# Performance work log

Measured on AMD Instinct MI355X. Metric: run time of the kernel, lower is better.

Reference implementation:

```python
import jax, jax.numpy as jnp
import numpy as np

B, C, H, W = 8, 256, 64, 64
D = C // 8  # qk proj dim = 32
R = C // 8  # channel-SE reduction dim = 32

def setup_inputs() -> dict:
    key = jax.random.key(0)
    ks = jax.random.split(key, 10)
    s = lambda *sh: 1.0 / np.sqrt(sh[-1])
    return {
        'x':  jax.random.normal(ks[0], (B, C, H, W), jnp.float32),
        'Wq': jax.random.normal(ks[1], (D, C), jnp.float32) * s(D, C),
        'bq': jnp.zeros((D,), jnp.float32),
        'Wk': jax.random.normal(ks[2], (D, C), jnp.float32) * s(D, C),
        'bk': jnp.zeros((D,), jnp.float32),
        'Wv': jax.random.normal(ks[3], (C, C), jnp.float32) * s(C, C),
        'bv': jnp.zeros((C,), jnp.float32),
        'gamma': jnp.ones((1,), jnp.float32),
        'W1': jax.random.normal(ks[4], (R, 2 * C), jnp.float32) * s(R, 2 * C),
        'W2': jax.random.normal(ks[5], (C, R), jnp.float32) * s(C, R),
        'lamb': jnp.ones((1,), jnp.float32),
    }

def reference(x, Wq, bq, Wk, bk, Wv, bv, gamma, W1, W2, lamb):
    b, c, h, w = x.shape
    n = h * w
    xf = x.reshape(b, c, n)  # [B,C,N]
    # --- spatial self-attention (1x1 convs == matmuls over channel dim) ---
    q = jnp.einsum('dc,bcn->bnd', Wq, xf) + bq            # [B,N,D]
    k = jnp.einsum('dc,bcn->bdn', Wk, xf) + bk[:, None]   # [B,D,N]
    attn = jax.nn.softmax(jnp.einsum('bnd,bdm->bnm', q, k), axis=-1)  # [B,N,N]
    v = jnp.einsum('dc,bcn->bdn', Wv, xf) + bv[:, None]   # [B,C,N]
    # out[b,c,m] = sum_n v[b,c,n] * attn[b,m,n]  (torch: bmm(v, attn^T))
    sp = jnp.einsum('bcn,bmn->bcm', v, attn).reshape(b, c, h, w)
    sp = gamma * sp
    # --- channel SE-gate ---
    mean = jnp.mean(xf, axis=-1)                # [B,C]
    std = jnp.std(xf, axis=-1, ddof=1)          # torch.std uses unbiased (ddof=1)
    inp = jnp.concatenate([mean, std], axis=1)  # [B,2C]
    a = jax.nn.sigmoid(jax.nn.relu(inp @ W1.T) @ W2.T)  # [B,C]
    ch = lamb * a[:, :, None, None] * x
    return sp + ch + x
```

## Files before the change

### kernel.cpp

```cpp
#include <hip/hip_runtime.h>
#include <hip/hip_bf16.h>

#define Bb 8
#define Cc 256
#define Nn 4096
#define Dd 32

typedef short bf16x8 __attribute__((ext_vector_type(8)));
typedef short bf16x4 __attribute__((ext_vector_type(4)));
typedef float f32x4 __attribute__((ext_vector_type(4)));
typedef unsigned int u32;

__device__ __forceinline__ void glds16(const void* g, void* l) {
    __builtin_amdgcn_global_load_lds(
        (const __attribute__((address_space(1))) unsigned int*)g,
        (__attribute__((address_space(3))) unsigned int*)l, 16, 0, 0);
}

__device__ __forceinline__ u32 pkbf16(float a, float b) {
    return ((u32)__bfloat16_as_ushort(__float2bfloat16(b)) << 16) |
           (u32)__bfloat16_as_ushort(__float2bfloat16(a));
}

__global__ __launch_bounds__(256) void convt_kernel(
    const float* __restrict__ x, __hip_bfloat16* __restrict__ x_t,
    float* __restrict__ sum_ws, float* __restrict__ sumsq_ws)
{
    __shared__ __hip_bfloat16 tile[64][68];
    const int n0 = blockIdx.x * 64, c0 = blockIdx.y * 64, b = blockIdx.z;
    const int t = threadIdx.x;

#pragma unroll
    for (int i = 0; i < 4; i++) {
        int id = i * 256 + t;
        int row = id >> 4, col4 = id & 15;
        float4 v = *(const float4*)(x + ((size_t)(b * Cc + c0 + row)) * Nn + n0 + col4 * 4);
        bf16x4 bv;
        bv[0] = __bfloat16_as_short(__float2bfloat16(v.x));
        bv[1] = __bfloat16_as_short(__float2bfloat16(v.y));
        bv[2] = __bfloat16_as_short(__float2bfloat16(v.z));
        bv[3] = __bfloat16_as_short(__float2bfloat16(v.w));
        *(bf16x4*)((void*)&tile[row][col4 * 4]) = bv;
        float ls  = v.x + v.y + v.z + v.w;
        float ls2 = v.x * v.x + v.y * v.y + v.z * v.z + v.w * v.w;
        ls  += __shfl_xor(ls, 1, 16);  ls2 += __shfl_xor(ls2, 1, 16);
        ls  += __shfl_xor(ls, 2, 16);  ls2 += __shfl_xor(ls2, 2, 16);
        ls  += __shfl_xor(ls, 4, 16);  ls2 += __shfl_xor(ls2, 4, 16);
        ls  += __shfl_xor(ls, 8, 16);  ls2 += __shfl_xor(ls2, 8, 16);
        if ((t & 15) == 0) {
            atomicAdd(&sum_ws[b * Cc + c0 + row], ls);
            atomicAdd(&sumsq_ws[b * Cc + c0 + row], ls2);
        }
    }
    __syncthreads();
#pragma unroll
    for (int i = 0; i < 2; i++) {
        int id = i * 256 + t;
        int nl = id >> 3, cg = id & 7;
        bf16x8 o;
#pragma unroll
        for (int j = 0; j < 8; j++) o[j] = __bfloat16_as_short(tile[cg * 8 + j][nl]);
        *(bf16x8*)(x_t + ((size_t)(b * Nn + n0 + nl)) * Cc + c0 + cg * 8) = o;
    }
}

__global__ __launch_bounds__(256) void wconv_kernel(
    const float* __restrict__ Wq, const float* __restrict__ Wk, const float* __restrict__ Wv,
    __hip_bfloat16* __restrict__ w_bf)
{
    const int ct = blockIdx.x;
    const int t = threadIdx.x;
#pragma unroll
    for (int i = 0; i < 8; i++) {
        int g = i * 256 + t;
        int row = g >> 5, c8 = g & 31;
        int c0 = c8 * 8;
        int grow = ct * 64 + row;
        const float* src;
        if (grow < 32)       src = Wq + (size_t)grow * Cc + c0;
        else if (grow < 64)  src = Wk + (size_t)(grow - 32) * Cc + c0;
        else                 src = Wv + (size_t)(grow - 64) * Cc + c0;
        float4 v0 = *(const float4*)src;
        float4 v1 = *(const float4*)(src + 4);
        bf16x8 o;
        o[0] = __bfloat16_as_short(__float2bfloat16(v0.x));
        o[1] = __bfloat16_as_short(__float2bfloat16(v0.y));
        o[2] = __bfloat16_as_short(__float2bfloat16(v0.z));
        o[3] = __bfloat16_as_short(__float2bfloat16(v0.w));
        o[4] = __bfloat16_as_short(__float2bfloat16(v1.x));
        o[5] = __bfloat16_as_short(__float2bfloat16(v1.y));
        o[6] = __bfloat16_as_short(__float2bfloat16(v1.z));
        o[7] = __bfloat16_as_short(__float2bfloat16(v1.w));
        int kchunk = c0 >> 5, qd = (c0 & 31) >> 3, cg = row >> 4, rl = row & 15;
        *(bf16x8*)(w_bf + ((size_t)ct * 32 + kchunk * 4 + cg) * 512 + (qd * 16 + rl) * 8) = o;
    }
}

__global__ __launch_bounds__(256, 2) void proj_kernel(
    const __hip_bfloat16* __restrict__ x_t, const __hip_bfloat16* __restrict__ w_bf,
    const float* __restrict__ bq, const float* __restrict__ bk, const float* __restrict__ bv,
    __hip_bfloat16* __restrict__ q_ws, __hip_bfloat16* __restrict__ k_ws,
    __hip_bfloat16* __restrict__ v_ws)
{
    __shared__ __hip_bfloat16 ldsX[32 * 512];
    __shared__ __hip_bfloat16 ldsW[32 * 512];

    const int n0 = blockIdx.x * 64;
    const int ct = blockIdx.y;
    const int b  = blockIdx.z;
    const int t = threadIdx.x;
    const int w = t >> 6, lane = t & 63, quad = lane >> 4, l15 = lane & 15;

#pragma unroll
    for (int j = 0; j < 8; j++) {
        int idx = w * 8 + j;
        int kchunk = idx >> 2, ngrp = idx & 3;
        glds16(x_t + ((size_t)(b * Nn + n0 + ngrp * 16 + l15)) * Cc + kchunk * 32 + quad * 8,
               ldsX + idx * 512);
        glds16(w_bf + ((size_t)ct * 32 + idx) * 512 + lane * 8, ldsW + idx * 512);
    }
    __syncthreads();

    f32x4 acc[4];
#pragma unroll
    for (int cg = 0; cg < 4; cg++) {
        int gcol = ct * 64 + cg * 16 + l15;
        float bias = (gcol < 32) ? bq[gcol] : (gcol < 64 ? bk[gcol - 32] : bv[gcol - 64]);
        acc[cg] = (f32x4){bias, bias, bias, bias};
    }

#pragma unroll
    for (int kchunk = 0; kchunk < 8; kchunk++) {
        bf16x8 a = *(const bf16x8*)(ldsX + ((kchunk * 4 + w) * 64 + lane) * 8);
#pragma unroll
        for (int cg = 0; cg < 4; cg++) {
            bf16x8 bw = *(const bf16x8*)(ldsW + ((kchunk * 4 + cg) * 64 + lane) * 8);
            acc[cg] = __builtin_amdgcn_mfma_f32_16x16x32_bf16(a, bw, acc[cg], 0, 0, 0);
        }
    }

#pragma unroll
    for (int cg = 0; cg < 4; cg++) {
        int gcol = ct * 64 + cg * 16 + l15;
        int nb = n0 + w * 16 + quad * 4;
        if (gcol < 64) {
            __hip_bfloat16* dst = (gcol < 32) ? q_ws : k_ws;
            int d = gcol & 31;
#pragma unroll
            for (int r = 0; r < 4; r++)
                dst[((size_t)(b * Nn + nb + r)) * Dd + d] = __float2bfloat16(acc[cg][r]);
        } else {
            int c = gcol - 64;
            bf16x4 o;
#pragma unroll
            for (int r = 0; r < 4; r++) o[r] = __bfloat16_as_short(__float2bfloat16(acc[cg][r]));
            *(bf16x4*)(v_ws + ((size_t)(b * Cc + c)) * Nn + nb) = o;
        }
    }
}

__global__ __launch_bounds__(256) void gate_kernel(
    const float* __restrict__ sum_ws, const float* __restrict__ sumsq_ws,
    const float* __restrict__ W1, const float* __restrict__ W2,
    const float* __restrict__ lamb, float* __restrict__ coef)
{
    int b = blockIdx.x;
    __shared__ float inp[2 * Cc];
    __shared__ float h[32];
    int t = threadIdx.x;
    float s  = sum_ws[b * Cc + t];
    float s2 = sumsq_ws[b * Cc + t];
    float m   = s / Nn;
    float var = (s2 - (float)Nn * m * m) / (float)(Nn - 1);
    inp[t]      = m;
    inp[Cc + t] = sqrtf(fmaxf(var, 0.f));
    __syncthreads();
    if (t < 32) {
        float a = 0.f;
        for (int i = 0; i < 2 * Cc; i++) a += W1[t * (2 * Cc) + i] * inp[i];
        h[t] = fmaxf(a, 0.f);
    }
    __syncthreads();
    float g = 0.f;
#pragma unroll
    for (int r = 0; r < 32; r++) g += W2[t * 32 + r] * h[r];
    float a = 1.f / (1.f + __expf(-g));
    coef[b * Cc + t] = 1.f + lamb[0] * a;
}

__global__ __launch_bounds__(512, 2) void attn_kernel(
    const __hip_bfloat16* __restrict__ q_ws, const __hip_bfloat16* __restrict__ k_ws,
    const __hip_bfloat16* __restrict__ v_ws, const float* __restrict__ coef,
    const float* __restrict__ x, const float* __restrict__ gamma_p,
    float* __restrict__ out)
{
    extern __shared__ __hip_bfloat16 smem[];
    __hip_bfloat16* vbuf0 = smem;
    __hip_bfloat16* vbuf1 = smem + 16384;
    __hip_bfloat16* kbuf0 = smem + 32768;
    __hip_bfloat16* kbuf1 = smem + 36864;

    const int b  = blockIdx.x & 7;
    const int m0 = (blockIdx.x >> 3) * 128;
    const int t = threadIdx.x;
    const int w = t >> 6, lane = t & 63, quad = lane >> 4, l15 = lane & 15;
    const int p = w >> 2, pw = w & 3;

    const bf16x8 aq0 = *(const bf16x8*)(q_ws + ((size_t)(b * Nn + m0 + (2 * pw)     * 16 + l15)) * Dd + quad * 8);
    const bf16x8 aq1 = *(const bf16x8*)(q_ws + ((size_t)(b * Nn + m0 + (2 * pw + 1) * 16 + l15)) * Dd + quad * 8);

    const __hip_bfloat16* vsrc[4];
#pragma unroll
    for (int j = 0; j < 4; j++) {
        int idx = w * 4 + j;
        int ch = idx >> 4, tc = idx & 15;
        vsrc[j] = v_ws + ((size_t)(b * Cc + tc * 16 + l15)) * Nn + ch * 32 + quad * 8;
    }
    const int sl15 = (l15 & 3) | ((l15 & 4) << 1) | ((l15 & 8) >> 1);
    const __hip_bfloat16* ksrc = k_ws + ((size_t)(b * Nn + w * 16 + sl15)) * Dd + quad * 8;

#pragma unroll
    for (int j = 0; j < 4; j++) glds16(vsrc[j], vbuf0 + (w * 4 + j) * 512);
    glds16(ksrc, kbuf0 + w * 512);
    __syncthreads();

    f32x4 acc[2][16];
#pragma unroll
    for (int i = 0; i < 2; i++)
#pragma unroll
        for (int j = 0; j < 16; j++) acc[i][j] = (f32x4){0.f, 0.f, 0.f, 0.f};
    float lsum0 = 0.f, lsum1 = 0.f;

    const int NIT = Nn / 64;

    u32 pc0[2][2], pc1[2][2];
#pragma unroll
    for (int j = 0; j < 2; j++) {
        bf16x8 ak = *(const bf16x8*)(kbuf0 + ((2 * p + j) * 64 + lane) * 8);
        f32x4 s0 = __builtin_amdgcn_mfma_f32_16x16x32_bf16(ak, aq0, (f32x4){0.f,0.f,0.f,0.f}, 0, 0, 0);
        f32x4 s1 = __builtin_amdgcn_mfma_f32_16x16x32_bf16(ak, aq1, (f32x4){0.f,0.f,0.f,0.f}, 0, 0, 0);
        float a0 = __expf(s0[0]), a1 = __expf(s0[1]), a2 = __expf(s0[2]), a3 = __expf(s0[3]);
        lsum0 += (a0 + a1) + (a2 + a3);
        pc0[j][0] = pkbf16(a0, a1); pc0[j][1] = pkbf16(a2, a3);
        float b0 = __expf(s1[0]), b1 = __expf(s1[1]), b2 = __expf(s1[2]), b3 = __expf(s1[3]);
        lsum1 += (b0 + b1) + (b2 + b3);
        pc1[j][0] = pkbf16(b0, b1); pc1[j][1] = pkbf16(b2, b3);
    }

    for (int it = 0; it < NIT; it++) {
        if (it + 1 < NIT) {
            __hip_bfloat16* vn = ((it + 1) & 1) ? vbuf1 : vbuf0;
#pragma unroll
            for (int j = 0; j < 4; j++)
                glds16(vsrc[j] + (size_t)(it + 1) * 64, vn + (w * 4 + j) * 512);
        }
        if ((it & 1) == 0 && it + 2 < NIT) {
            int sl = (it >> 1) + 1;
            glds16(ksrc + (size_t)(sl * 128) * Dd, ((sl & 1) ? kbuf1 : kbuf0) + w * 512);
        }

        auto g0 = __builtin_amdgcn_permlane32_swap(pc0[0][0], pc0[1][0], false, false);
        auto g1 = __builtin_amdgcn_permlane32_swap(pc0[0][1], pc0[1][1], false, false);
        auto h0 = __builtin_amdgcn_permlane32_swap(pc1[0][0], pc1[1][0], false, false);
        auto h1 = __builtin_amdgcn_permlane32_swap(pc1[0][1], pc1[1][1], false, false);
        union { u32 uw[4]; bf16x8 v; } bp0, bp1;
        bp0.uw[0] = g0[0]; bp0.uw[1] = g1[0]; bp0.uw[2] = g0[1]; bp0.uw[3] = g1[1];
        bp1.uw[0] = h0[0]; bp1.uw[1] = h1[0]; bp1.uw[2] = h0[1]; bp1.uw[3] = h1[1];

        u32 pn0[2][2], pn1[2][2];
        const int itn = (it + 1 < NIT) ? it + 1 : it;
        const __hip_bfloat16* kbn = (((itn >> 1) & 1) ? kbuf1 : kbuf0) + (itn & 1) * 2048;
        float nls0 = 0.f, nls1 = 0.f;
#pragma unroll
        for (int j = 0; j < 2; j++) {
            bf16x8 ak = *(const bf16x8*)(kbn + ((2 * p + j) * 64 + lane) * 8);
            f32x4 s0 = __builtin_amdgcn_mfma_f32_16x16x32_bf16(ak, aq0, (f32x4){0.f,0.f,0.f,0.f}, 0, 0, 0);
            f32x4 s1 = __builtin_amdgcn_mfma_f32_16x16x32_bf16(ak, aq1, (f32x4){0.f,0.f,0.f,0.f}, 0, 0, 0);
            float a0 = __expf(s0[0]), a1 = __expf(s0[1]), a2 = __expf(s0[2]), a3 = __expf(s0[3]);
            nls0 += (a0 + a1) + (a2 + a3);
            pn0[j][0] = pkbf16(a0, a1); pn0[j][1] = pkbf16(a2, a3);
            float b0 = __expf(s1[0]), b1 = __expf(s1[1]), b2 = __expf(s1[2]), b3 = __expf(s1[3]);
            nls1 += (b0 + b1) + (b2 + b3);
            pn1[j][0] = pkbf16(b0, b1); pn1[j][1] = pkbf16(b2, b3);
        }
        if (it + 1 < NIT) { lsum0 += nls0; lsum1 += nls1; }

        const __hip_bfloat16* vb = (it & 1) ? vbuf1 : vbuf0;
#pragma unroll
        for (int cf = 0; cf < 16; cf++) {
            bf16x8 av = *(const bf16x8*)(vb + ((p * 16 + cf) * 64 + lane) * 8);
            acc[0][cf] = __builtin_amdgcn_mfma_f32_16x16x32_bf16(av, bp0.v, acc[0][cf], 0, 0, 0);
            acc[1][cf] = __builtin_amdgcn_mfma_f32_16x16x32_bf16(av, bp1.v, acc[1][cf], 0, 0, 0);
        }

#pragma unroll
        for (int j = 0; j < 2; j++)
#pragma unroll
            for (int k = 0; k < 2; k++) { pc0[j][k] = pn0[j][k]; pc1[j][k] = pn1[j][k]; }

        __syncthreads();
    }

    float* lex = (float*)(smem + 32768);
    lex[w * 128 + lane]      = lsum0;
    lex[w * 128 + 64 + lane] = lsum1;
    f32x4* exv = (f32x4*)smem;
#pragma unroll
    for (int mfi = 0; mfi < 2; mfi++) {
        __syncthreads();
        if (p == 0) {
#pragma unroll
            for (int j = 0; j < 8; j++) exv[(w * 8 + j) * 64 + lane] = acc[mfi][8 + j];
        } else {
#pragma unroll
            for (int j = 0; j < 8; j++) exv[(w * 8 + j) * 64 + lane] = acc[mfi][j];
        }
        __syncthreads();
        if (p == 0) {
#pragma unroll
            for (int j = 0; j < 8; j++) acc[mfi][j] += exv[((w ^ 4) * 8 + j) * 64 + lane];
        } else {
#pragma unroll
            for (int j = 0; j < 8; j++) acc[mfi][8 + j] += exv[((w ^ 4) * 8 + j) * 64 + lane];
        }
        if (mfi == 0) {
            lsum0 += lex[(w ^ 4) * 128 + lane];
            lsum1 += lex[(w ^ 4) * 128 + 64 + lane];
        }
    }

    lsum0 += __shfl_xor(lsum0, 16); lsum0 += __shfl_xor(lsum0, 32);
    lsum1 += __shfl_xor(lsum1, 16); lsum1 += __shfl_xor(lsum1, 32);
    const float g = gamma_p[0];
    const float inv0 = g / lsum0, inv1 = g / lsum1;

    if (p == 0) {
#pragma unroll
        for (int j = 0; j < 8; j++) {
#pragma unroll
            for (int r = 0; r < 4; r++) {
                int c = j * 16 + quad * 4 + r;
                float cfv = coef[b * Cc + c];
                size_t base = ((size_t)(b * Cc + c)) * Nn + m0 + (2 * pw) * 16 + l15;
                out[base]      = acc[0][j][r] * inv0 + cfv * x[base];
                out[base + 16] = acc[1][j][r] * inv1 + cfv * x[base + 16];
            }
        }
    } else {
#pragma unroll
        for (int j = 0; j < 8; j++) {
#pragma unroll
            for (int r = 0; r < 4; r++) {
                int c = (8 + j) * 16 + quad * 4 + r;
                float cfv = coef[b * Cc + c];
                size_t base = ((size_t)(b * Cc + c)) * Nn + m0 + (2 * pw) * 16 + l15;
                out[base]      = acc[0][8 + j][r] * inv0 + cfv * x[base];
                out[base + 16] = acc[1][8 + j][r] * inv1 + cfv * x[base + 16];
            }
        }
    }
}

extern "C" void kernel_launch(void* const* d_in, const int* in_sizes, int n_in,
                              void* d_out, int out_size, void* d_ws, size_t ws_size,
                              hipStream_t stream) {
    const float* x     = (const float*)d_in[0];
    const float* Wq    = (const float*)d_in[1];
    const float* bq    = (const float*)d_in[2];
    const float* Wk    = (const float*)d_in[3];
    const float* bk    = (const float*)d_in[4];
    const float* Wv    = (const float*)d_in[5];
    const float* bv    = (const float*)d_in[6];
    const float* gamma = (const float*)d_in[7];
    const float* W1    = (const float*)d_in[8];
    const float* W2    = (const float*)d_in[9];
    const float* lamb  = (const float*)d_in[10];
    float* out = (float*)d_out;

    char* ws = (char*)d_ws;
    __hip_bfloat16* q_ws = (__hip_bfloat16*)ws;
    __hip_bfloat16* k_ws = (__hip_bfloat16*)(ws + (2u  << 20));
    __hip_bfloat16* v_ws = (__hip_bfloat16*)(ws + (4u  << 20));
    __hip_bfloat16* x_t  = (__hip_bfloat16*)(ws + (20u << 20));
    float* sum_ws   = (float*)(ws + (36u << 20));
    float* sumsq_ws = sum_ws + Bb * Cc;
    float* coef     = sumsq_ws + Bb * Cc;
    __hip_bfloat16* w_bf = (__hip_bfloat16*)(ws + (37u << 20));

    (void)hipFuncSetAttribute((const void*)attn_kernel,
                              hipFuncAttributeMaxDynamicSharedMemorySize, 81920);

    hipMemsetAsync(sum_ws, 0, 2 * Bb * Cc * sizeof(float), stream);
    wconv_kernel<<<5, 256, 0, stream>>>(Wq, Wk, Wv, w_bf);
    convt_kernel<<<dim3(Nn / 64, Cc / 64, Bb), 256, 0, stream>>>(x, x_t, sum_ws, sumsq_ws);
    proj_kernel<<<dim3(Nn / 64, 5, Bb), 256, 0, stream>>>(x_t, w_bf, bq, bk, bv, q_ws, k_ws, v_ws);
    gate_kernel<<<Bb, 256, 0, stream>>>(sum_ws, sumsq_ws, W1, W2, lamb, coef);
    attn_kernel<<<256, 512, 81920, stream>>>(q_ws, k_ws, v_ws, coef, x, gamma, out);
}
```

Baseline: 245.7 us.

## Triple-buffer V/K tiles in attention loop with prefetch distance two

The attention kernel's V and K shared-memory staging moves from double to triple buffering with rotating pointers, so global-to-LDS loads are issued two iterations ahead. The per-iteration __syncthreads is replaced by an explicit s_waitcnt vmcnt(4) plus s_barrier, so the most recent prefetch can stay in flight across the barrier. The aim is to hide global memory latency behind the MFMA work. In exchange, dynamic LDS per block rises from 80 KB to 120 KB, which rules out two resident blocks per CU, and correctness now depends on the hand-written waitcnt counting.

```diff
diff --git a/kernel.cpp b/kernel.cpp
--- a/kernel.cpp
+++ b/kernel.cpp
@@ -195,10 +195,8 @@
     float* __restrict__ out)
 {
     extern __shared__ __hip_bfloat16 smem[];
-    __hip_bfloat16* vbuf0 = smem;
-    __hip_bfloat16* vbuf1 = smem + 16384;
-    __hip_bfloat16* kbuf0 = smem + 32768;
-    __hip_bfloat16* kbuf1 = smem + 36864;
+    __hip_bfloat16 *vcur = smem, *vnext = smem + 16384, *vnn = smem + 32768;
+    __hip_bfloat16 *kA = smem + 49152, *kB = smem + 53248, *kC = smem + 57344;
 
     const int b  = blockIdx.x & 7;
     const int m0 = (blockIdx.x >> 3) * 128;
@@ -220,8 +218,11 @@
     const __hip_bfloat16* ksrc = k_ws + ((size_t)(b * Nn + w * 16 + sl15)) * Dd + quad * 8;
 
 #pragma unroll
-    for (int j = 0; j < 4; j++) glds16(vsrc[j], vbuf0 + (w * 4 + j) * 512);
-    glds16(ksrc, kbuf0 + w * 512);
+    for (int j = 0; j < 4; j++) glds16(vsrc[j], vcur + (w * 4 + j) * 512);
+#pragma unroll
+    for (int j = 0; j < 4; j++) glds16(vsrc[j] + 64, vnext + (w * 4 + j) * 512);
+    glds16(ksrc, kA + w * 512);
+    glds16(ksrc + (size_t)128 * Dd, kB + w * 512);
     __syncthreads();
 
     f32x4 acc[2][16];
@@ -236,7 +237,7 @@
     u32 pc0[2][2], pc1[2][2];
 #pragma unroll
     for (int j = 0; j < 2; j++) {
-        bf16x8 ak = *(const bf16x8*)(kbuf0 + ((2 * p + j) * 64 + lane) * 8);
+        bf16x8 ak = *(const bf16x8*)(kA + ((2 * p + j) * 64 + lane) * 8);
         f32x4 s0 = __builtin_amdgcn_mfma_f32_16x16x32_bf16(ak, aq0, (f32x4){0.f,0.f,0.f,0.f}, 0, 0, 0);
         f32x4 s1 = __builtin_amdgcn_mfma_f32_16x16x32_bf16(ak, aq1, (f32x4){0.f,0.f,0.f,0.f}, 0, 0, 0);
         float a0 = __expf(s0[0]), a1 = __expf(s0[1]), a2 = __expf(s0[2]), a3 = __expf(s0[3]);
@@ -248,16 +249,13 @@
     }
 
     for (int it = 0; it < NIT; it++) {
-        if (it + 1 < NIT) {
-            __hip_bfloat16* vn = ((it + 1) & 1) ? vbuf1 : vbuf0;
+        if (it + 2 < NIT) {
 #pragma unroll
             for (int j = 0; j < 4; j++)
-                glds16(vsrc[j] + (size_t)(it + 1) * 64, vn + (w * 4 + j) * 512);
-        }
-        if ((it & 1) == 0 && it + 2 < NIT) {
-            int sl = (it >> 1) + 1;
-            glds16(ksrc + (size_t)(sl * 128) * Dd, ((sl & 1) ? kbuf1 : kbuf0) + w * 512);
-        }
+                glds16(vsrc[j] + (size_t)(it + 2) * 64, vnn + (w * 4 + j) * 512);
+        }
+        if ((it & 1) == 0 && (it >> 1) + 2 < 32)
+            glds16(ksrc + (size_t)(((it >> 1) + 2) * 128) * Dd, kC + w * 512);
 
         auto g0 = __builtin_amdgcn_permlane32_swap(pc0[0][0], pc0[1][0], false, false);
         auto g1 = __builtin_amdgcn_permlane32_swap(pc0[0][1], pc0[1][1], false, false);
@@ -268,12 +266,12 @@
         bp1.uw[0] = h0[0]; bp1.uw[1] = h1[0]; bp1.uw[2] = h0[1]; bp1.uw[3] = h1[1];
 
         u32 pn0[2][2], pn1[2][2];
-        const int itn = (it + 1 < NIT) ? it + 1 : it;
-        const __hip_bfloat16* kbn = (((itn >> 1) & 1) ? kbuf1 : kbuf0) + (itn & 1) * 2048;
+        const int itn = (it + 1 < NIT) ? it + 1 : NIT - 1;
+        const __hip_bfloat16* kb = (((itn >> 1) > (it >> 1)) ? kB : kA) + (itn & 1) * 2048;
         float nls0 = 0.f, nls1 = 0.f;
 #pragma unroll
         for (int j = 0; j < 2; j++) {
-            bf16x8 ak = *(const bf16x8*)(kbn + ((2 * p + j) * 64 + lane) * 8);
+            bf16x8 ak = *(const bf16x8*)(kb + ((2 * p + j) * 64 + lane) * 8);
             f32x4 s0 = __builtin_amdgcn_mfma_f32_16x16x32_bf16(ak, aq0, (f32x4){0.f,0.f,0.f,0.f}, 0, 0, 0);
             f32x4 s1 = __builtin_amdgcn_mfma_f32_16x16x32_bf16(ak, aq1, (f32x4){0.f,0.f,0.f,0.f}, 0, 0, 0);
             float a0 = __expf(s0[0]), a1 = __expf(s0[1]), a2 = __expf(s0[2]), a3 = __expf(s0[3]);
@@ -285,10 +283,9 @@
         }
         if (it + 1 < NIT) { lsum0 += nls0; lsum1 += nls1; }
 
-        const __hip_bfloat16* vb = (it & 1) ? vbuf1 : vbuf0;
 #pragma unroll
         for (int cf = 0; cf < 16; cf++) {
-            bf16x8 av = *(const bf16x8*)(vb + ((p * 16 + cf) * 64 + lane) * 8);
+            bf16x8 av = *(const bf16x8*)(vcur + ((p * 16 + cf) * 64 + lane) * 8);
             acc[0][cf] = __builtin_amdgcn_mfma_f32_16x16x32_bf16(av, bp0.v, acc[0][cf], 0, 0, 0);
             acc[1][cf] = __builtin_amdgcn_mfma_f32_16x16x32_bf16(av, bp1.v, acc[1][cf], 0, 0, 0);
         }
@@ -298,7 +295,13 @@
 #pragma unroll
             for (int k = 0; k < 2; k++) { pc0[j][k] = pn0[j][k]; pc1[j][k] = pn1[j][k]; }
 
-        __syncthreads();
+        { __hip_bfloat16* vt = vcur; vcur = vnext; vnext = vnn; vnn = vt; }
+        if (it & 1) { __hip_bfloat16* kt = kA; kA = kB; kB = kC; kC = kt; }
+
+        if (it + 2 < NIT)
+            asm volatile("s_waitcnt vmcnt(4)\n\ts_barrier" ::: "memory");
+        else
+            asm volatile("s_waitcnt vmcnt(0)\n\ts_barrier" ::: "memory");
     }
 
     float* lex = (float*)(smem + 32768);
@@ -388,12 +391,12 @@
     __hip_bfloat16* w_bf = (__hip_bfloat16*)(ws + (37u << 20));
 
     (void)hipFuncSetAttribute((const void*)attn_kernel,
-                              hipFuncAttributeMaxDynamicSharedMemorySize, 81920);
+                              hipFuncAttributeMaxDynamicSharedMemorySize, 122880);
 
     hipMemsetAsync(sum_ws, 0, 2 * Bb * Cc * sizeof(float), stream);
     wconv_kernel<<<5, 256, 0, stream>>>(Wq, Wk, Wv, w_bf);
     convt_kernel<<<dim3(Nn / 64, Cc / 64, Bb), 256, 0, stream>>>(x, x_t, sum_ws, sumsq_ws);
     proj_kernel<<<dim3(Nn / 64, 5, Bb), 256, 0, stream>>>(x_t, w_bf, bq, bk, bv, q_ws, k_ws, v_ws);
     gate_kernel<<<Bb, 256, 0, stream>>>(sum_ws, sumsq_ws, W1, W2, lamb, coef);
-    attn_kernel<<<256, 512, 81920, stream>>>(q_ws, k_ws, v_ws, coef, x, gamma, out);
-}
+    attn_kernel<<<256, 512, 122880, stream>>>(q_ws, k_ws, v_ws, coef, x, gamma, out);
+}
```

Result: faster. 235.6 us (-4.1%).
